# Kernel optimization log

Hardware: AMD Instinct MI355X
Metric: run time of the kernel (lower is better)

## Reference

```python
import jax, jax.numpy as jnp
import numpy as np

B, N, C = 2, 9216, 512
HEAD, SR = 8, 4
R = 32  # lora rank
SCALING = 4.0 / 32.0  # alpha / r


def setup_inputs() -> dict:
    key = jax.random.key(0)
    ks = jax.random.split(key, 16)
    s = 0.02
    inp = {
        "x": jax.random.normal(ks[0], (B, N, C), jnp.float32),
        "w_q": jax.random.normal(ks[1], (C, C), jnp.float32) * s,
        "b_q": jnp.zeros((C,), jnp.float32),
        "w_kv": jax.random.normal(ks[2], (2 * C, C), jnp.float32) * s,
        "b_kv": jnp.zeros((2 * C,), jnp.float32),
        "w_proj": jax.random.normal(ks[3], (C, C), jnp.float32) * s,
        "b_proj": jnp.zeros((C,), jnp.float32),
        "w_sr": jax.random.normal(ks[4], (C, C, SR, SR), jnp.float32) * s,
        "b_sr": jnp.zeros((C,), jnp.float32),
        "ln_g": jnp.ones((C,), jnp.float32),
        "ln_b": jnp.zeros((C,), jnp.float32),
        "lora_A_q": jax.random.normal(ks[5], (R, C), jnp.float32) * s,
        "lora_B_q": jax.random.normal(ks[6], (C, R), jnp.float32) * s,
        "lora_A_v": jax.random.normal(ks[7], (R, C), jnp.float32) * s,
        "lora_B_v": jax.random.normal(ks[8], (C, R), jnp.float32) * s,
        "H": 96,
        "W": 96,
    }
    return inp


def reference(x, w_q, b_q, w_kv, b_kv, w_proj, b_proj, w_sr, b_sr,
              ln_g, ln_b, lora_A_q, lora_B_q, lora_A_v, lora_B_v, H, W):
    b, n, c = x.shape
    d = c // HEAD
    # q = Linear(x) + LoRA(x) * scaling
    q = x @ w_q.T + b_q + ((x @ lora_A_q.T) @ lora_B_q.T) * SCALING
    q = q.reshape(b, n, HEAD, d).transpose(0, 2, 1, 3)  # (B, h, N, d)
    # spatial reduction: Conv2d(dim, dim, sr, sr) then LayerNorm
    xi = x.transpose(0, 2, 1).reshape(b, c, H, W)
    xs = jax.lax.conv_general_dilated(
        xi, w_sr, window_strides=(SR, SR), padding='VALID',
        dimension_numbers=('NCHW', 'OIHW', 'NCHW'))
    xs = xs + b_sr[None, :, None, None]
    xs = xs.reshape(b, c, -1).transpose(0, 2, 1)  # (B, Nkv, C)
    mu = jnp.mean(xs, axis=-1, keepdims=True)
    var = jnp.var(xs, axis=-1, keepdims=True)
    xs = (xs - mu) * jax.lax.rsqrt(var + 1e-5) * ln_g + ln_b
    # k, v
    kv = (xs @ w_kv.T + b_kv).reshape(b, -1, 2, HEAD, d).transpose(2, 0, 3, 1, 4)
    k, v = kv[0], kv[1]  # (B, h, Nkv, d)
    lv = ((xs @ lora_A_v.T) @ lora_B_v.T) * SCALING  # (B, Nkv, C)
    # faithful to torch: raw memory reshape, NOT a head-transpose
    v = v + lv.reshape(b, HEAD, -1, d)
    # attention
    attn = jax.nn.softmax(jnp.einsum('bhnd,bhmd->bhnm', q, k) * (d ** -0.5), axis=-1)
    out = jnp.einsum('bhnm,bhmd->bhnd', attn, v).transpose(0, 2, 1, 3).reshape(b, n, c)
    return out @ w_proj.T + b_proj
```

## Files before the change

kernel.cpp:

```cpp
#include <hip/hip_runtime.h>

typedef __attribute__((ext_vector_type(8))) __bf16 bf16x8;
typedef __attribute__((ext_vector_type(4))) float f32x4;
typedef __attribute__((ext_vector_type(4))) unsigned int u32x4;
typedef __attribute__((ext_vector_type(2))) unsigned int u32x2;

#define MFMA16(a, b, c) __builtin_amdgcn_mfma_f32_16x16x32_bf16((a), (b), (c), 0, 0, 0)
#define QSCALE 0.18033688011112042f

__device__ __forceinline__ bool input_is_f32(const void* ln_g) {
    return ((const unsigned*)ln_g)[0] == 0x3F800000u;
}

__device__ __forceinline__ float rdf(const void* p, long i, bool f32) {
    return f32 ? ((const float*)p)[i] : (float)((const __bf16*)p)[i];
}

__device__ __forceinline__ void conv_big(const void* s, __bf16* d, long base, bool f) {
    long i = base + (long)threadIdx.x * 8;
    if (f) {
        f32x4 a = ((const f32x4*)s)[i / 4];
        f32x4 b = ((const f32x4*)s)[i / 4 + 1];
        bf16x8 o;
        #pragma unroll
        for (int j = 0; j < 4; ++j) { o[j] = (__bf16)a[j]; o[4 + j] = (__bf16)b[j]; }
        *(bf16x8*)(d + i) = o;
    } else {
        *(u32x4*)(d + i) = ((const u32x4*)s)[i / 8];
    }
}

__device__ __forceinline__ void conv_small(const void* s, __bf16* d, int n, bool f) {
    int i = threadIdx.x * 4;
    if (i < n) {
        #pragma unroll
        for (int j = 0; j < 4; ++j)
            d[i + j] = f ? (__bf16)((const float*)s)[i + j] : ((const __bf16*)s)[i + j];
    }
}

__global__ void convert_kernel(const void* x, const void* w_kv, const void* w_proj,
                               const void* b_q, const void* b_kv, const void* b_proj,
                               const void* b_sr, const void* ln_g, const void* ln_b,
                               __bf16* x_b, __bf16* w_kv_b, __bf16* w_proj_b,
                               __bf16* b_q_b, __bf16* b_kv_b, __bf16* b_proj_b,
                               __bf16* b_sr_b, __bf16* ln_g_b, __bf16* ln_b_b) {
    const bool f = input_is_f32(ln_g);
    int blk = blockIdx.x;
    if (blk < 4608)      conv_big(x, x_b, (long)blk * 2048, f);
    else if (blk < 4864) conv_big(w_kv, w_kv_b, (long)(blk - 4608) * 2048, f);
    else if (blk < 4992) conv_big(w_proj, w_proj_b, (long)(blk - 4864) * 2048, f);
    else if (blk == 4992) conv_small(b_q, b_q_b, 512, f);
    else if (blk == 4993) conv_small(b_kv, b_kv_b, 1024, f);
    else if (blk == 4994) conv_small(b_proj, b_proj_b, 512, f);
    else if (blk == 4995) conv_small(b_sr, b_sr_b, 512, f);
    else if (blk == 4996) conv_small(ln_g, ln_g_b, 512, f);
    else                  conv_small(ln_b, ln_b_b, 512, f);
}

__global__ void prep_kernel(const void* __restrict__ w_q,
                            const void* __restrict__ Aq, const void* __restrict__ Bq,
                            const void* __restrict__ Av, const void* __restrict__ Bv,
                            const void* __restrict__ w_sr, const void* __restrict__ ln_g,
                            __bf16* __restrict__ w_q_eff, __bf16* __restrict__ w_lv,
                            __bf16* __restrict__ w_sr_t) {
    const bool f = input_is_f32(ln_g);
    int tid = blockIdx.x * 256 + threadIdx.x;
    if (tid < 262144) {
        int o = tid >> 9, c = tid & 511;
        float acc = 0.f;
        #pragma unroll 8
        for (int r = 0; r < 32; ++r)
            acc += rdf(Bq, o * 32 + r, f) * rdf(Aq, r * 512 + c, f);
        w_q_eff[tid] = (__bf16)(rdf(w_q, tid, f) + 0.125f * acc);
    } else if (tid < 524288) {
        int t = tid - 262144;
        int o = t >> 9, c = t & 511;
        float acc = 0.f;
        #pragma unroll 8
        for (int r = 0; r < 32; ++r)
            acc += rdf(Bv, o * 32 + r, f) * rdf(Av, r * 512 + c, f);
        w_lv[t] = (__bf16)(0.125f * acc);
    } else if (tid < 786432) {
        int t = tid - 524288;
        int o = t >> 9, i = t & 511;
        #pragma unroll
        for (int p = 0; p < 16; ++p)
            w_sr_t[(size_t)o * 8192 + p * 512 + i] = (__bf16)rdf(w_sr, (long)t * 16 + p, f);
    }
}

__global__ __launch_bounds__(256) void gemm128(const __bf16* __restrict__ A,
                                               const __bf16* __restrict__ Bt,
                                               const __bf16* __restrict__ bias,
                                               void* __restrict__ out, int mode) {
    __shared__ __attribute__((aligned(16))) char lds[16384];
    char* As = lds;
    char* Bs = lds + 8192;
    const int tid = threadIdx.x;
    const int m0 = blockIdx.x << 7, n0 = blockIdx.y << 7;
    const int w = tid >> 6, lane = tid & 63;
    const int wm = (w >> 1) << 6, wn = (w & 1) << 6;
    const int lr = lane & 15, lg = lane >> 4;

    f32x4 acc[4][4] = {};

    const int srow = tid >> 1;
    const int sc0 = (tid & 1) * 2;
    const __bf16* Arow = A + (size_t)(m0 + srow) * 512;
    const __bf16* Brow = Bt + (size_t)(n0 + srow) * 512;

    for (int k0 = 0; k0 < 512; k0 += 32) {
        u32x4 a0 = *(const u32x4*)(Arow + k0 + sc0 * 8);
        u32x4 a1 = *(const u32x4*)(Arow + k0 + sc0 * 8 + 8);
        u32x4 b0 = *(const u32x4*)(Brow + k0 + sc0 * 8);
        u32x4 b1 = *(const u32x4*)(Brow + k0 + sc0 * 8 + 8);
        __syncthreads();
        *(u32x4*)(As + srow * 64 + sc0 * 16) = a0;
        *(u32x4*)(As + srow * 64 + sc0 * 16 + 16) = a1;
        *(u32x4*)(Bs + srow * 64 + sc0 * 16) = b0;
        *(u32x4*)(Bs + srow * 64 + sc0 * 16 + 16) = b1;
        __syncthreads();
        bf16x8 a[4], b[4];
        #pragma unroll
        for (int i = 0; i < 4; ++i)
            a[i] = *(const bf16x8*)(As + (wm + i * 16 + lr) * 64 + lg * 16);
        #pragma unroll
        for (int j = 0; j < 4; ++j)
            b[j] = *(const bf16x8*)(Bs + (wn + j * 16 + lr) * 64 + lg * 16);
        #pragma unroll
        for (int i = 0; i < 4; ++i)
            #pragma unroll
            for (int j = 0; j < 4; ++j)
                acc[i][j] = MFMA16(a[i], b[j], acc[i][j]);
    }

    #pragma unroll
    for (int j = 0; j < 4; ++j) {
        int col = n0 + wn + j * 16 + lr;
        float bv = (float)bias[col];
        #pragma unroll
        for (int i = 0; i < 4; ++i) {
            int rb = m0 + wm + i * 16 + lg * 4;
            #pragma unroll
            for (int r = 0; r < 4; ++r) {
                float v = acc[i][j][r] + bv;
                int grow = rb + r;
                if (mode == 0) {
                    ((float*)out)[(size_t)grow * 512 + col] = v;
                } else {
                    int b_ = grow >= 9216 ? 1 : 0;
                    int nn = grow - b_ * 9216;
                    ((__bf16*)out)[(((size_t)(b_ * 8 + (col >> 6))) * 9216 + nn) * 64 +
                                   (col & 63)] = (__bf16)(v * QSCALE);
                }
            }
        }
    }
}

__global__ __launch_bounds__(256) void conv_gemm(const __bf16* __restrict__ x,
                                                 const __bf16* __restrict__ Wt,
                                                 float* __restrict__ part) {
    __shared__ __attribute__((aligned(16))) char lds[18432];
    char* As = lds;
    char* Bs = lds + 9216;
    const int tid = threadIdx.x;
    const int m0 = blockIdx.x << 6, n0 = blockIdx.y << 6;
    const int kz = blockIdx.z;
    const int kbase = kz << 10;
    const int w = tid >> 6, lane = tid & 63;
    const int wm = (w >> 1) << 5, wn = (w & 1) << 5;
    const int lr = lane & 15, lg = lane >> 4;

    const int srow = tid >> 2, sc = tid & 3;
    int m = m0 + srow;
    int bb = m >= 576 ? 1 : 0;
    int rem = m - bb * 576;
    int oy = rem / 24;
    int ox = rem - oy * 24;
    const __bf16* xrow = x + ((size_t)bb * 9216 + oy * 384 + ox * 4) * 512;
    const __bf16* brow = Wt + (size_t)(n0 + srow) * 8192;

    f32x4 acc[2][2] = {};
    for (int kk = 0; kk < 1024; kk += 64) {
        int k0 = kbase + kk;
        int p = k0 >> 9;
        int i0 = k0 & 511;
        int ky = p >> 2, kx = p & 3;
        const __bf16* xsrc = xrow + ((ky * 96 + kx) << 9) + i0;
        __syncthreads();
        #pragma unroll
        for (int j = 0; j < 2; ++j) {
            int c = sc + j * 4;
            u32x4 av = *(const u32x4*)(xsrc + c * 8);
            u32x4 bv = *(const u32x4*)(brow + k0 + c * 8);
            *(u32x4*)(As + srow * 144 + c * 16) = av;
            *(u32x4*)(Bs + srow * 144 + c * 16) = bv;
        }
        __syncthreads();
        bf16x8 a[2][2], b[2][2];
        #pragma unroll
        for (int i = 0; i < 2; ++i)
            #pragma unroll
            for (int ks = 0; ks < 2; ++ks) {
                a[i][ks] = *(const bf16x8*)(As + (wm + i * 16 + lr) * 144 + ks * 64 + lg * 16);
                b[i][ks] = *(const bf16x8*)(Bs + (wn + i * 16 + lr) * 144 + ks * 64 + lg * 16);
            }
        #pragma unroll
        for (int i = 0; i < 2; ++i)
            #pragma unroll
            for (int j = 0; j < 2; ++j)
                #pragma unroll
                for (int ks = 0; ks < 2; ++ks)
                    acc[i][j] = MFMA16(a[i][ks], b[j][ks], acc[i][j]);
    }
    float* pout = part + (size_t)kz * 589824;
    #pragma unroll
    for (int j = 0; j < 2; ++j) {
        int col = n0 + wn + j * 16 + lr;
        #pragma unroll
        for (int i = 0; i < 2; ++i) {
            int rb = m0 + wm + i * 16 + lg * 4;
            #pragma unroll
            for (int r = 0; r < 4; ++r)
                pout[(size_t)(rb + r) * 512 + col] = acc[i][j][r];
        }
    }
}

__global__ __launch_bounds__(64) void lnorm(const float* __restrict__ parts,
                                            const __bf16* __restrict__ b_sr,
                                            const __bf16* __restrict__ g,
                                            const __bf16* __restrict__ be,
                                            __bf16* __restrict__ out) {
    int row = blockIdx.x;
    int lane = threadIdx.x;
    const float* xr = parts + (size_t)row * 512;
    float v[8], s = 0.f, sq = 0.f;
    #pragma unroll
    for (int i = 0; i < 8; ++i) {
        int c = lane + i * 64;
        float t = (float)b_sr[c];
        #pragma unroll
        for (int sp = 0; sp < 8; ++sp)
            t += xr[(size_t)sp * 589824 + c];
        v[i] = t;
        s += t;
        sq += t * t;
    }
    #pragma unroll
    for (int d = 1; d < 64; d <<= 1) {
        s += __shfl_xor(s, d);
        sq += __shfl_xor(sq, d);
    }
    float mean = s * (1.0f / 512.0f);
    float var = sq * (1.0f / 512.0f) - mean * mean;
    float rstd = rsqrtf(var + 1e-5f);
    __bf16* orow = out + (size_t)row * 512;
    #pragma unroll
    for (int i = 0; i < 8; ++i) {
        int c = lane + i * 64;
        orow[c] = (__bf16)((v[i] - mean) * rstd * (float)g[c] + (float)be[c]);
    }
}

__global__ __launch_bounds__(256) void kv_gemm(const __bf16* __restrict__ xs,
                                               const __bf16* __restrict__ w_kv,
                                               const __bf16* __restrict__ w_lv,
                                               const __bf16* __restrict__ b_kv,
                                               __bf16* __restrict__ k_t,
                                               float* __restrict__ v_raw,
                                               __bf16* __restrict__ lv) {
    __shared__ __attribute__((aligned(16))) char lds[18432];
    char* As = lds;
    char* Bs = lds + 9216;
    const int tid = threadIdx.x;
    const int m0 = blockIdx.x << 6, n0 = blockIdx.y << 6;
    const int w = tid >> 6, lane = tid & 63;
    const int wm = (w >> 1) << 5, wn = (w & 1) << 5;
    const int lr = lane & 15, lg = lane >> 4;

    const int srow = tid >> 2, sc = tid & 3;
    const __bf16* arow = xs + (size_t)(m0 + srow) * 512;
    const __bf16* brow = (n0 < 1024) ? (w_kv + (size_t)(n0 + srow) * 512)
                                     : (w_lv + (size_t)(n0 - 1024 + srow) * 512);

    f32x4 acc[2][2] = {};
    for (int k0 = 0; k0 < 512; k0 += 64) {
        __syncthreads();
        #pragma unroll
        for (int j = 0; j < 2; ++j) {
            int c = sc + j * 4;
            u32x4 av = *(const u32x4*)(arow + k0 + c * 8);
            u32x4 bv = *(const u32x4*)(brow + k0 + c * 8);
            *(u32x4*)(As + srow * 144 + c * 16) = av;
            *(u32x4*)(Bs + srow * 144 + c * 16) = bv;
        }
        __syncthreads();
        bf16x8 a[2][2], b[2][2];
        #pragma unroll
        for (int i = 0; i < 2; ++i)
            #pragma unroll
            for (int ks = 0; ks < 2; ++ks) {
                a[i][ks] = *(const bf16x8*)(As + (wm + i * 16 + lr) * 144 + ks * 64 + lg * 16);
                b[i][ks] = *(const bf16x8*)(Bs + (wn + i * 16 + lr) * 144 + ks * 64 + lg * 16);
            }
        #pragma unroll
        for (int i = 0; i < 2; ++i)
            #pragma unroll
            for (int j = 0; j < 2; ++j)
                #pragma unroll
                for (int ks = 0; ks < 2; ++ks)
                    acc[i][j] = MFMA16(a[i][ks], b[j][ks], acc[i][j]);
    }
    #pragma unroll
    for (int j = 0; j < 2; ++j) {
        int col = n0 + wn + j * 16 + lr;
        float bv = (col < 1024) ? (float)b_kv[col] : 0.0f;
        #pragma unroll
        for (int i = 0; i < 2; ++i) {
            int rb = m0 + wm + i * 16 + lg * 4;
            #pragma unroll
            for (int r = 0; r < 4; ++r) {
                int grow = rb + r;
                float val = acc[i][j][r] + bv;
                int b_ = grow >= 576 ? 1 : 0;
                int mm = grow - b_ * 576;
                if (col < 512) {
                    int h = col >> 6, dd = col & 63;
                    k_t[(((size_t)(b_ * 8 + h)) * 576 + mm) * 64 + dd] = (__bf16)val;
                } else if (col < 1024) {
                    v_raw[((size_t)b_ * 576 + mm) * 512 + (col - 512)] = val;
                } else {
                    lv[((size_t)b_ * 576 + mm) * 512 + (col - 1024)] = (__bf16)val;
                }
            }
        }
    }
}

__global__ void v_fixup(const float* __restrict__ v_raw, const __bf16* __restrict__ lv,
                        __bf16* __restrict__ vT) {
    int tid = blockIdx.x * 256 + threadIdx.x;
    if (tid >= 589824) return;
    int mm = tid % 576;
    int rest = tid / 576;
    int dd = rest & 63;
    int bh = rest >> 6;
    int b_ = bh >> 3, h = bh & 7;
    int flat = h * 36864 + mm * 64 + dd;
    int n2 = flat >> 9, c2 = flat & 511;
    float val = v_raw[((size_t)b_ * 576 + mm) * 512 + h * 64 + dd] +
                (float)lv[((size_t)b_ * 576 + n2) * 512 + c2];
    vT[tid] = (__bf16)val;
}

__global__ __launch_bounds__(256) void attn_kernel(const __bf16* __restrict__ q_t,
                                                   const __bf16* __restrict__ k_t,
                                                   const __bf16* __restrict__ vT,
                                                   __bf16* __restrict__ attnv) {
    __shared__ __attribute__((aligned(16))) char lds[18432];
    char* Ks = lds;
    char* Vs = lds + 9216;
    const int tid = threadIdx.x;
    const int w = tid >> 6, lane = tid & 63;
    const int lr = lane & 15, lg = lane >> 4;
    const int bh = blockIdx.y;
    const int qrow0 = (blockIdx.x << 7) + (w << 5);

    bf16x8 qf[2][2];
    #pragma unroll
    for (int qb = 0; qb < 2; ++qb)
        #pragma unroll
        for (int ks = 0; ks < 2; ++ks)
            qf[qb][ks] = *(const bf16x8*)(q_t + ((size_t)bh * 9216 + qrow0 + qb * 16 + lr) * 64 +
                                          ks * 32 + lg * 8);

    bf16x8 ones;
    #pragma unroll
    for (int j = 0; j < 8; ++j) ones[j] = (__bf16)1.0f;

    f32x4 oacc[2][4] = {};
    f32x4 lacc[2] = {};

    const int rr = tid >> 2, q4 = tid & 3;
    const __bf16* kg = k_t + ((size_t)bh * 576 + rr) * 64 + q4 * 16;
    char* ksw = Ks + rr * 144 + q4 * 32;
    const __bf16* vg = vT + ((size_t)bh * 64 + rr) * 576 + q4 * 16;
    char* vsw = Vs + rr * 144;
    const int offA = ((q4 & 1) << 3) | ((q4 >> 1) << 6);

    for (int kv0 = 0; kv0 < 576; kv0 += 64) {
        u32x4 k0v = *(const u32x4*)(kg + (size_t)kv0 * 64);
        u32x4 k1v = *(const u32x4*)(kg + (size_t)kv0 * 64 + 8);
        u32x4 v0v = *(const u32x4*)(vg + kv0);
        u32x4 v1v = *(const u32x4*)(vg + kv0 + 8);
        __syncthreads();
        *(u32x4*)(ksw) = k0v;
        *(u32x4*)(ksw + 16) = k1v;
        u32x2 t0, t1, t2, t3;
        t0[0] = v0v[0]; t0[1] = v0v[1];
        t1[0] = v0v[2]; t1[1] = v0v[3];
        t2[0] = v1v[0]; t2[1] = v1v[1];
        t3[0] = v1v[2]; t3[1] = v1v[3];
        *(u32x2*)(vsw + offA) = t0;
        *(u32x2*)(vsw + offA + 16) = t1;
        *(u32x2*)(vsw + offA + 32) = t2;
        *(u32x2*)(vsw + offA + 48) = t3;
        __syncthreads();

        #pragma unroll
        for (int ch = 0; ch < 2; ++ch) {
            bf16x8 kf[2][2];
            #pragma unroll
            for (int kb = 0; kb < 2; ++kb)
                #pragma unroll
                for (int ks = 0; ks < 2; ++ks)
                    kf[kb][ks] = *(const bf16x8*)(Ks + ((ch * 2 + kb) * 16 + lr) * 144 +
                                                  ks * 64 + lg * 16);
            f32x4 st[2][2] = {};
            #pragma unroll
            for (int kb = 0; kb < 2; ++kb)
                #pragma unroll
                for (int qb = 0; qb < 2; ++qb)
                    #pragma unroll
                    for (int ks = 0; ks < 2; ++ks)
                        st[kb][qb] = MFMA16(kf[kb][ks], qf[qb][ks], st[kb][qb]);
            bf16x8 vf[4];
            #pragma unroll
            for (int nd = 0; nd < 4; ++nd)
                vf[nd] = *(const bf16x8*)(Vs + (nd * 16 + lr) * 144 + ch * 64 + lg * 16);
            #pragma unroll
            for (int qb = 0; qb < 2; ++qb) {
                bf16x8 pa;
                #pragma unroll
                for (int kb = 0; kb < 2; ++kb)
                    #pragma unroll
                    for (int r = 0; r < 4; ++r)
                        pa[kb * 4 + r] = (__bf16)__builtin_amdgcn_exp2f(st[kb][qb][r]);
                #pragma unroll
                for (int nd = 0; nd < 4; ++nd)
                    oacc[qb][nd] = MFMA16(pa, vf[nd], oacc[qb][nd]);
                lacc[qb] = MFMA16(pa, ones, lacc[qb]);
            }
        }
    }

    const int b_ = bh >> 3, h = bh & 7;
    #pragma unroll
    for (int qb = 0; qb < 2; ++qb) {
        f32x4 linv;
        #pragma unroll
        for (int r = 0; r < 4; ++r) linv[r] = 1.0f / lacc[qb][r];
        #pragma unroll
        for (int nd = 0; nd < 4; ++nd)
            #pragma unroll
            for (int r = 0; r < 4; ++r) {
                int row = qrow0 + qb * 16 + lg * 4 + r;
                int col = h * 64 + nd * 16 + lr;
                attnv[((size_t)b_ * 9216 + row) * 512 + col] =
                    (__bf16)(oacc[qb][nd][r] * linv[r]);
            }
    }
}

extern "C" void kernel_launch(void* const* d_in, const int* in_sizes, int n_in,
                              void* d_out, int out_size, void* d_ws, size_t ws_size,
                              hipStream_t stream) {
    const void* x      = d_in[0];
    const void* w_q    = d_in[1];
    const void* b_q    = d_in[2];
    const void* w_kv   = d_in[3];
    const void* b_kv   = d_in[4];
    const void* w_proj = d_in[5];
    const void* b_proj = d_in[6];
    const void* w_sr   = d_in[7];
    const void* b_sr   = d_in[8];
    const void* ln_g   = d_in[9];
    const void* ln_b   = d_in[10];
    const void* A_q    = d_in[11];
    const void* B_q    = d_in[12];
    const void* A_v    = d_in[13];
    const void* B_v    = d_in[14];

    char* ws = (char*)d_ws;
    __bf16* x_b      = (__bf16*)(ws);
    __bf16* attnv    = (__bf16*)(ws);
    float*  parts    = (float*)(ws + 18874368);
    __bf16* q_t      = (__bf16*)(ws + 18874368);
    __bf16* k_t      = (__bf16*)(ws + 37748736);
    __bf16* vT       = (__bf16*)(ws + 38928384);
    __bf16* w_q_eff  = (__bf16*)(ws + 40108032);
    __bf16* w_lv     = (__bf16*)(ws + 40632320);
    __bf16* w_sr_t   = (__bf16*)(ws + 41156608);
    __bf16* w_kv_b   = (__bf16*)(ws + 49545216);
    __bf16* w_proj_b = (__bf16*)(ws + 50593792);
    __bf16* xs_ln    = (__bf16*)(ws + 53477376);
    float*  v_raw    = (float*)(ws + 54657024);
    __bf16* lv       = (__bf16*)(ws + 57016320);
    __bf16* b_q_b    = (__bf16*)(ws + 58195968);
    __bf16* b_kv_b   = (__bf16*)(ws + 58196992);
    __bf16* b_proj_b = (__bf16*)(ws + 58199040);
    __bf16* b_sr_b   = (__bf16*)(ws + 58200064);
    __bf16* ln_g_b   = (__bf16*)(ws + 58201088);
    __bf16* ln_b_b   = (__bf16*)(ws + 58202112);

    convert_kernel<<<4998, 256, 0, stream>>>(x, w_kv, w_proj, b_q, b_kv, b_proj,
                                             b_sr, ln_g, ln_b,
                                             x_b, w_kv_b, w_proj_b, b_q_b, b_kv_b,
                                             b_proj_b, b_sr_b, ln_g_b, ln_b_b);
    prep_kernel<<<3072, 256, 0, stream>>>(w_q, A_q, B_q, A_v, B_v, w_sr, ln_g,
                                          w_q_eff, w_lv, w_sr_t);
    conv_gemm<<<dim3(18, 8, 8), 256, 0, stream>>>(x_b, w_sr_t, parts);
    lnorm<<<1152, 64, 0, stream>>>(parts, b_sr_b, ln_g_b, ln_b_b, xs_ln);
    gemm128<<<dim3(144, 4), 256, 0, stream>>>(x_b, w_q_eff, b_q_b, q_t, 1);
    kv_gemm<<<dim3(18, 24), 256, 0, stream>>>(xs_ln, w_kv_b, w_lv, b_kv_b, k_t, v_raw, lv);
    v_fixup<<<2304, 256, 0, stream>>>(v_raw, lv, vT);
    attn_kernel<<<dim3(72, 16), 256, 0, stream>>>(q_t, k_t, vT, attnv);
    gemm128<<<dim3(144, 4), 256, 0, stream>>>(attnv, w_proj_b, b_proj_b, d_out, 0);
}
```

Baseline: 269.9 us.

## Merge convert and prep kernels, widen GEMM K-tile, give attention warps 64 query rows

The convert and weight-prep kernels are merged into one launch with a combined block range. The 128x128 GEMM now stages a 64-wide K slice per iteration into padded LDS rows (144-byte stride), which halves the number of barriers and is meant to reduce bank conflicts. The attention kernel drops to 128 threads, with each warp handling 64 query rows instead of 32, so each K/V tile loaded into LDS is reused across more queries. The cost is higher register pressure in attention (four times the accumulators per warp) and more LDS per GEMM block, both of which may lower occupancy.

```diff
diff --git a/kernel.cpp b/kernel.cpp
--- a/kernel.cpp
+++ b/kernel.cpp
@@ -39,12 +39,18 @@
     }
 }
 
-__global__ void convert_kernel(const void* x, const void* w_kv, const void* w_proj,
-                               const void* b_q, const void* b_kv, const void* b_proj,
-                               const void* b_sr, const void* ln_g, const void* ln_b,
-                               __bf16* x_b, __bf16* w_kv_b, __bf16* w_proj_b,
-                               __bf16* b_q_b, __bf16* b_kv_b, __bf16* b_proj_b,
-                               __bf16* b_sr_b, __bf16* ln_g_b, __bf16* ln_b_b) {
+__global__ void convert_prep_kernel(const void* x, const void* w_kv, const void* w_proj,
+                                    const void* b_q, const void* b_kv, const void* b_proj,
+                                    const void* b_sr, const void* ln_g, const void* ln_b,
+                                    const void* __restrict__ w_q,
+                                    const void* __restrict__ Aq, const void* __restrict__ Bq,
+                                    const void* __restrict__ Av, const void* __restrict__ Bv,
+                                    const void* __restrict__ w_sr,
+                                    __bf16* x_b, __bf16* w_kv_b, __bf16* w_proj_b,
+                                    __bf16* b_q_b, __bf16* b_kv_b, __bf16* b_proj_b,
+                                    __bf16* b_sr_b, __bf16* ln_g_b, __bf16* ln_b_b,
+                                    __bf16* __restrict__ w_q_eff, __bf16* __restrict__ w_lv,
+                                    __bf16* __restrict__ w_sr_t) {
     const bool f = input_is_f32(ln_g);
     int blk = blockIdx.x;
     if (blk < 4608)      conv_big(x, x_b, (long)blk * 2048, f);
@@ -55,38 +61,31 @@
     else if (blk == 4994) conv_small(b_proj, b_proj_b, 512, f);
     else if (blk == 4995) conv_small(b_sr, b_sr_b, 512, f);
     else if (blk == 4996) conv_small(ln_g, ln_g_b, 512, f);
-    else                  conv_small(ln_b, ln_b_b, 512, f);
-}
-
-__global__ void prep_kernel(const void* __restrict__ w_q,
-                            const void* __restrict__ Aq, const void* __restrict__ Bq,
-                            const void* __restrict__ Av, const void* __restrict__ Bv,
-                            const void* __restrict__ w_sr, const void* __restrict__ ln_g,
-                            __bf16* __restrict__ w_q_eff, __bf16* __restrict__ w_lv,
-                            __bf16* __restrict__ w_sr_t) {
-    const bool f = input_is_f32(ln_g);
-    int tid = blockIdx.x * 256 + threadIdx.x;
-    if (tid < 262144) {
-        int o = tid >> 9, c = tid & 511;
-        float acc = 0.f;
-        #pragma unroll 8
-        for (int r = 0; r < 32; ++r)
-            acc += rdf(Bq, o * 32 + r, f) * rdf(Aq, r * 512 + c, f);
-        w_q_eff[tid] = (__bf16)(rdf(w_q, tid, f) + 0.125f * acc);
-    } else if (tid < 524288) {
-        int t = tid - 262144;
-        int o = t >> 9, c = t & 511;
-        float acc = 0.f;
-        #pragma unroll 8
-        for (int r = 0; r < 32; ++r)
-            acc += rdf(Bv, o * 32 + r, f) * rdf(Av, r * 512 + c, f);
-        w_lv[t] = (__bf16)(0.125f * acc);
-    } else if (tid < 786432) {
-        int t = tid - 524288;
-        int o = t >> 9, i = t & 511;
-        #pragma unroll
-        for (int p = 0; p < 16; ++p)
-            w_sr_t[(size_t)o * 8192 + p * 512 + i] = (__bf16)rdf(w_sr, (long)t * 16 + p, f);
+    else if (blk == 4997) conv_small(ln_b, ln_b_b, 512, f);
+    else {
+        int tid = (blk - 4998) * 256 + threadIdx.x;
+        if (tid < 262144) {
+            int o = tid >> 9, c = tid & 511;
+            float acc = 0.f;
+            #pragma unroll 8
+            for (int r = 0; r < 32; ++r)
+                acc += rdf(Bq, o * 32 + r, f) * rdf(Aq, r * 512 + c, f);
+            w_q_eff[tid] = (__bf16)(rdf(w_q, tid, f) + 0.125f * acc);
+        } else if (tid < 524288) {
+            int t = tid - 262144;
+            int o = t >> 9, c = t & 511;
+            float acc = 0.f;
+            #pragma unroll 8
+            for (int r = 0; r < 32; ++r)
+                acc += rdf(Bv, o * 32 + r, f) * rdf(Av, r * 512 + c, f);
+            w_lv[t] = (__bf16)(0.125f * acc);
+        } else if (tid < 786432) {
+            int t = tid - 524288;
+            int o = t >> 9, i = t & 511;
+            #pragma unroll
+            for (int p = 0; p < 16; ++p)
+                w_sr_t[(size_t)o * 8192 + p * 512 + i] = (__bf16)rdf(w_sr, (long)t * 16 + p, f);
+        }
     }
 }
 
@@ -94,9 +93,9 @@
                                                const __bf16* __restrict__ Bt,
                                                const __bf16* __restrict__ bias,
                                                void* __restrict__ out, int mode) {
-    __shared__ __attribute__((aligned(16))) char lds[16384];
+    __shared__ __attribute__((aligned(16))) char lds[36864];
     char* As = lds;
-    char* Bs = lds + 8192;
+    char* Bs = lds + 18432;
     const int tid = threadIdx.x;
     const int m0 = blockIdx.x << 7, n0 = blockIdx.y << 7;
     const int w = tid >> 6, lane = tid & 63;
@@ -106,33 +105,49 @@
     f32x4 acc[4][4] = {};
 
     const int srow = tid >> 1;
-    const int sc0 = (tid & 1) * 2;
-    const __bf16* Arow = A + (size_t)(m0 + srow) * 512;
-    const __bf16* Brow = Bt + (size_t)(n0 + srow) * 512;
-
-    for (int k0 = 0; k0 < 512; k0 += 32) {
-        u32x4 a0 = *(const u32x4*)(Arow + k0 + sc0 * 8);
-        u32x4 a1 = *(const u32x4*)(Arow + k0 + sc0 * 8 + 8);
-        u32x4 b0 = *(const u32x4*)(Brow + k0 + sc0 * 8);
-        u32x4 b1 = *(const u32x4*)(Brow + k0 + sc0 * 8 + 8);
-        __syncthreads();
-        *(u32x4*)(As + srow * 64 + sc0 * 16) = a0;
-        *(u32x4*)(As + srow * 64 + sc0 * 16 + 16) = a1;
-        *(u32x4*)(Bs + srow * 64 + sc0 * 16) = b0;
-        *(u32x4*)(Bs + srow * 64 + sc0 * 16 + 16) = b1;
-        __syncthreads();
-        bf16x8 a[4], b[4];
+    const int half = tid & 1;
+    const __bf16* Arow = A + (size_t)(m0 + srow) * 512 + half * 32;
+    const __bf16* Brow = Bt + (size_t)(n0 + srow) * 512 + half * 32;
+    char* Asw = As + srow * 144 + half * 64;
+    char* Bsw = Bs + srow * 144 + half * 64;
+
+    for (int k0 = 0; k0 < 512; k0 += 64) {
+        u32x4 a0 = *(const u32x4*)(Arow + k0);
+        u32x4 a1 = *(const u32x4*)(Arow + k0 + 8);
+        u32x4 a2 = *(const u32x4*)(Arow + k0 + 16);
+        u32x4 a3 = *(const u32x4*)(Arow + k0 + 24);
+        u32x4 b0 = *(const u32x4*)(Brow + k0);
+        u32x4 b1 = *(const u32x4*)(Brow + k0 + 8);
+        u32x4 b2 = *(const u32x4*)(Brow + k0 + 16);
+        u32x4 b3 = *(const u32x4*)(Brow + k0 + 24);
+        __syncthreads();
+        *(u32x4*)(Asw) = a0;
+        *(u32x4*)(Asw + 16) = a1;
+        *(u32x4*)(Asw + 32) = a2;
+        *(u32x4*)(Asw + 48) = a3;
+        *(u32x4*)(Bsw) = b0;
+        *(u32x4*)(Bsw + 16) = b1;
+        *(u32x4*)(Bsw + 32) = b2;
+        *(u32x4*)(Bsw + 48) = b3;
+        __syncthreads();
+        bf16x8 a[4][2], b[4][2];
         #pragma unroll
         for (int i = 0; i < 4; ++i)
-            a[i] = *(const bf16x8*)(As + (wm + i * 16 + lr) * 64 + lg * 16);
+            #pragma unroll
+            for (int ks = 0; ks < 2; ++ks)
+                a[i][ks] = *(const bf16x8*)(As + (wm + i * 16 + lr) * 144 + ks * 64 + lg * 16);
         #pragma unroll
         for (int j = 0; j < 4; ++j)
-            b[j] = *(const bf16x8*)(Bs + (wn + j * 16 + lr) * 64 + lg * 16);
+            #pragma unroll
+            for (int ks = 0; ks < 2; ++ks)
+                b[j][ks] = *(const bf16x8*)(Bs + (wn + j * 16 + lr) * 144 + ks * 64 + lg * 16);
         #pragma unroll
         for (int i = 0; i < 4; ++i)
             #pragma unroll
             for (int j = 0; j < 4; ++j)
-                acc[i][j] = MFMA16(a[i], b[j], acc[i][j]);
+                #pragma unroll
+                for (int ks = 0; ks < 2; ++ks)
+                    acc[i][j] = MFMA16(a[i][ks], b[j][ks], acc[i][j]);
     }
 
     #pragma unroll
@@ -356,10 +371,10 @@
     vT[tid] = (__bf16)val;
 }
 
-__global__ __launch_bounds__(256) void attn_kernel(const __bf16* __restrict__ q_t,
-                                                   const __bf16* __restrict__ k_t,
-                                                   const __bf16* __restrict__ vT,
-                                                   __bf16* __restrict__ attnv) {
+__global__ __launch_bounds__(128, 2) void attn_kernel(const __bf16* __restrict__ q_t,
+                                                      const __bf16* __restrict__ k_t,
+                                                      const __bf16* __restrict__ vT,
+                                                      __bf16* __restrict__ attnv) {
     __shared__ __attribute__((aligned(16))) char lds[18432];
     char* Ks = lds;
     char* Vs = lds + 9216;
@@ -367,11 +382,11 @@
     const int w = tid >> 6, lane = tid & 63;
     const int lr = lane & 15, lg = lane >> 4;
     const int bh = blockIdx.y;
-    const int qrow0 = (blockIdx.x << 7) + (w << 5);
-
-    bf16x8 qf[2][2];
-    #pragma unroll
-    for (int qb = 0; qb < 2; ++qb)
+    const int qrow0 = (blockIdx.x << 7) + (w << 6);
+
+    bf16x8 qf[4][2];
+    #pragma unroll
+    for (int qb = 0; qb < 4; ++qb)
         #pragma unroll
         for (int ks = 0; ks < 2; ++ks)
             qf[qb][ks] = *(const bf16x8*)(q_t + ((size_t)bh * 9216 + qrow0 + qb * 16 + lr) * 64 +
@@ -381,33 +396,50 @@
     #pragma unroll
     for (int j = 0; j < 8; ++j) ones[j] = (__bf16)1.0f;
 
-    f32x4 oacc[2][4] = {};
-    f32x4 lacc[2] = {};
-
-    const int rr = tid >> 2, q4 = tid & 3;
-    const __bf16* kg = k_t + ((size_t)bh * 576 + rr) * 64 + q4 * 16;
-    char* ksw = Ks + rr * 144 + q4 * 32;
-    const __bf16* vg = vT + ((size_t)bh * 64 + rr) * 576 + q4 * 16;
+    f32x4 oacc[4][4] = {};
+    f32x4 lacc[4] = {};
+
+    const int rr = tid >> 1, hc = tid & 1;
+    const __bf16* kg = k_t + ((size_t)bh * 576 + rr) * 64 + hc * 32;
+    char* ksw = Ks + rr * 144 + hc * 64;
+    const __bf16* vg = vT + ((size_t)bh * 64 + rr) * 576 + hc * 32;
     char* vsw = Vs + rr * 144;
-    const int offA = ((q4 & 1) << 3) | ((q4 >> 1) << 6);
 
     for (int kv0 = 0; kv0 < 576; kv0 += 64) {
         u32x4 k0v = *(const u32x4*)(kg + (size_t)kv0 * 64);
         u32x4 k1v = *(const u32x4*)(kg + (size_t)kv0 * 64 + 8);
+        u32x4 k2v = *(const u32x4*)(kg + (size_t)kv0 * 64 + 16);
+        u32x4 k3v = *(const u32x4*)(kg + (size_t)kv0 * 64 + 24);
         u32x4 v0v = *(const u32x4*)(vg + kv0);
         u32x4 v1v = *(const u32x4*)(vg + kv0 + 8);
+        u32x4 v2v = *(const u32x4*)(vg + kv0 + 16);
+        u32x4 v3v = *(const u32x4*)(vg + kv0 + 24);
         __syncthreads();
         *(u32x4*)(ksw) = k0v;
         *(u32x4*)(ksw + 16) = k1v;
-        u32x2 t0, t1, t2, t3;
-        t0[0] = v0v[0]; t0[1] = v0v[1];
-        t1[0] = v0v[2]; t1[1] = v0v[3];
-        t2[0] = v1v[0]; t2[1] = v1v[1];
-        t3[0] = v1v[2]; t3[1] = v1v[3];
-        *(u32x2*)(vsw + offA) = t0;
-        *(u32x2*)(vsw + offA + 16) = t1;
-        *(u32x2*)(vsw + offA + 32) = t2;
-        *(u32x2*)(vsw + offA + 48) = t3;
+        *(u32x4*)(ksw + 32) = k2v;
+        *(u32x4*)(ksw + 48) = k3v;
+        {
+            u32x2 t0, t1, t2, t3;
+            t0[0] = v0v[0]; t0[1] = v0v[1];
+            t1[0] = v0v[2]; t1[1] = v0v[3];
+            t2[0] = v1v[0]; t2[1] = v1v[1];
+            t3[0] = v1v[2]; t3[1] = v1v[3];
+            char* p = vsw + (hc << 6);
+            *(u32x2*)(p) = t0;
+            *(u32x2*)(p + 16) = t1;
+            *(u32x2*)(p + 32) = t2;
+            *(u32x2*)(p + 48) = t3;
+            t0[0] = v2v[0]; t0[1] = v2v[1];
+            t1[0] = v2v[2]; t1[1] = v2v[3];
+            t2[0] = v3v[0]; t2[1] = v3v[1];
+            t3[0] = v3v[2]; t3[1] = v3v[3];
+            p += 8;
+            *(u32x2*)(p) = t0;
+            *(u32x2*)(p + 16) = t1;
+            *(u32x2*)(p + 32) = t2;
+            *(u32x2*)(p + 48) = t3;
+        }
         __syncthreads();
 
         #pragma unroll
@@ -419,11 +451,11 @@
                 for (int ks = 0; ks < 2; ++ks)
                     kf[kb][ks] = *(const bf16x8*)(Ks + ((ch * 2 + kb) * 16 + lr) * 144 +
                                                   ks * 64 + lg * 16);
-            f32x4 st[2][2] = {};
+            f32x4 st[2][4] = {};
             #pragma unroll
             for (int kb = 0; kb < 2; ++kb)
                 #pragma unroll
-                for (int qb = 0; qb < 2; ++qb)
+                for (int qb = 0; qb < 4; ++qb)
                     #pragma unroll
                     for (int ks = 0; ks < 2; ++ks)
                         st[kb][qb] = MFMA16(kf[kb][ks], qf[qb][ks], st[kb][qb]);
@@ -432,7 +464,7 @@
             for (int nd = 0; nd < 4; ++nd)
                 vf[nd] = *(const bf16x8*)(Vs + (nd * 16 + lr) * 144 + ch * 64 + lg * 16);
             #pragma unroll
-            for (int qb = 0; qb < 2; ++qb) {
+            for (int qb = 0; qb < 4; ++qb) {
                 bf16x8 pa;
                 #pragma unroll
                 for (int kb = 0; kb < 2; ++kb)
@@ -449,7 +481,7 @@
 
     const int b_ = bh >> 3, h = bh & 7;
     #pragma unroll
-    for (int qb = 0; qb < 2; ++qb) {
+    for (int qb = 0; qb < 4; ++qb) {
         f32x4 linv;
         #pragma unroll
         for (int r = 0; r < 4; ++r) linv[r] = 1.0f / lacc[qb][r];
@@ -506,17 +538,16 @@
     __bf16* ln_g_b   = (__bf16*)(ws + 58201088);
     __bf16* ln_b_b   = (__bf16*)(ws + 58202112);
 
-    convert_kernel<<<4998, 256, 0, stream>>>(x, w_kv, w_proj, b_q, b_kv, b_proj,
-                                             b_sr, ln_g, ln_b,
-                                             x_b, w_kv_b, w_proj_b, b_q_b, b_kv_b,
-                                             b_proj_b, b_sr_b, ln_g_b, ln_b_b);
-    prep_kernel<<<3072, 256, 0, stream>>>(w_q, A_q, B_q, A_v, B_v, w_sr, ln_g,
-                                          w_q_eff, w_lv, w_sr_t);
+    convert_prep_kernel<<<8070, 256, 0, stream>>>(
+        x, w_kv, w_proj, b_q, b_kv, b_proj, b_sr, ln_g, ln_b,
+        w_q, A_q, B_q, A_v, B_v, w_sr,
+        x_b, w_kv_b, w_proj_b, b_q_b, b_kv_b, b_proj_b, b_sr_b, ln_g_b, ln_b_b,
+        w_q_eff, w_lv, w_sr_t);
     conv_gemm<<<dim3(18, 8, 8), 256, 0, stream>>>(x_b, w_sr_t, parts);
     lnorm<<<1152, 64, 0, stream>>>(parts, b_sr_b, ln_g_b, ln_b_b, xs_ln);
     gemm128<<<dim3(144, 4), 256, 0, stream>>>(x_b, w_q_eff, b_q_b, q_t, 1);
     kv_gemm<<<dim3(18, 24), 256, 0, stream>>>(xs_ln, w_kv_b, w_lv, b_kv_b, k_t, v_raw, lv);
     v_fixup<<<2304, 256, 0, stream>>>(v_raw, lv, vT);
-    attn_kernel<<<dim3(72, 16), 256, 0, stream>>>(q_t, k_t, vT, attnv);
+    attn_kernel<<<dim3(72, 16), 128, 0, stream>>>(q_t, k_t, vT, attnv);
     gemm128<<<dim3(144, 4), 256, 0, stream>>>(attnv, w_proj_b, b_proj_b, d_out, 0);
 }
```

After: 267.7 us. About the same (-0.8%).
